# Performance work log

Hardware: AMD Instinct MI355X
Metric: run time of the kernel (lower is better)

## Reference

```python
import jax, jax.numpy as jnp
import numpy as np

IN_FEATURES = 4096
OUT_FEATURES = 11008
LUT_SIZE = 256
N_TOKENS = 64


def setup_inputs() -> dict:
    key = jax.random.key(0)
    k1, k2, k3, k4 = jax.random.split(key, 4)
    x = jax.random.normal(k1, (N_TOKENS, IN_FEATURES), dtype=jnp.float32)
    grid_indices = jax.random.randint(k2, (OUT_FEATURES, IN_FEATURES), 0, LUT_SIZE, dtype=jnp.int32)
    lut = jax.random.normal(k3, (LUT_SIZE,), dtype=jnp.float32)
    scale = jax.random.uniform(k4, (OUT_FEATURES, 1), dtype=jnp.float32)
    return {"x": x, "grid_indices": grid_indices, "lut": lut, "scale": scale}


def reference(x, grid_indices, lut, scale):
    # Dequantize weight: LUT gather per element, then per-output-row scale.
    # weight: [out_features, in_features]
    weight = lut[grid_indices] * scale
    # F.linear(x, W) == x @ W.T ; out: [n_tokens, out_features]
    return jnp.einsum('ti,oi->to', x, weight)
```

## Files before the change

### kernel.cpp

```cpp
#include <hip/hip_runtime.h>
#include <stdint.h>

#define N_TOK 64
#define K_DIM 4096
#define N_OUT 11008
#define LUT_N 256

typedef __attribute__((ext_vector_type(4))) float  floatx4;
typedef __attribute__((ext_vector_type(8))) __bf16 bf16x8;

__device__ __forceinline__ unsigned bf16_rne(float f) {
  unsigned u = __builtin_bit_cast(unsigned, f);
  return (u + 0x7fffu + ((u >> 16) & 1u)) >> 16;
}

__global__ __launch_bounds__(256) void xpack_kernel(const float* __restrict__ x,
                                                    uint32_t* __restrict__ xp) {
  const int t = blockIdx.x * 256 + threadIdx.x;
  const int lane = t & 63, c = t >> 6;
  const int m15 = lane & 15, q = lane >> 4;
  const int tt = c & 3, st = (c >> 2) & 31, w = c >> 7;
  const int src = (tt * 16 + m15) * K_DIM + w * 1024 + st * 32 + q * 8;
  float4 a = *(const float4*)(x + src);
  float4 b = *(const float4*)(x + src + 4);
  uint4 o;
  o.x = bf16_rne(a.x) | (bf16_rne(a.y) << 16);
  o.y = bf16_rne(a.z) | (bf16_rne(a.w) << 16);
  o.z = bf16_rne(b.x) | (bf16_rne(b.y) << 16);
  o.w = bf16_rne(b.z) | (bf16_rne(b.w) << 16);
  *(uint4*)(xp + (size_t)t * 4) = o;
}

__global__ __launch_bounds__(256, 3) void ghost_kernel(
    const int* __restrict__ gidx, const float* __restrict__ lut,
    const float* __restrict__ scale, const uint32_t* __restrict__ xp,
    float* __restrict__ out) {
  __shared__ unsigned lut_lds[LUT_N * 16];
  __shared__ floatx4 red[4][4][64];

  const int tid = threadIdx.x;
  {
    unsigned hb = bf16_rne(lut[tid]);
#pragma unroll
    for (int c = 0; c < 16; ++c) lut_lds[tid * 16 + c] = hb;
  }
  __syncthreads();

  const int w = tid >> 6, lane = tid & 63;
  const int m15 = lane & 15, q = lane >> 4;
  const int o = blockIdx.x * 16 + m15;

  const int* idxp = gidx + (size_t)o * K_DIM + w * 1024 + q * 8;
  const uint4* ap = (const uint4*)xp + (size_t)w * 32 * 4 * 64 + lane;

  floatx4 acc[4];
#pragma unroll
  for (int tt = 0; tt < 4; ++tt) acc[tt] = (floatx4){0.f, 0.f, 0.f, 0.f};

  int4  ib[4][2];
  uint4 ab[4][4];
#pragma unroll
  for (int p = 0; p < 4; ++p) {
    ib[p][0] = *(const int4*)(idxp + p * 32);
    ib[p][1] = *(const int4*)(idxp + p * 32 + 4);
#pragma unroll
    for (int tt = 0; tt < 4; ++tt) ab[p][tt] = ap[(p * 4 + tt) * 64];
  }

#pragma unroll 4
  for (int st = 0; st < 32; ++st) {
    const int p = st & 3;
    const int4 i0 = ib[p][0], i1 = ib[p][1];
    uint4 a0 = ab[p][0], a1 = ab[p][1], a2 = ab[p][2], a3 = ab[p][3];
    if (st < 28) {
      ib[p][0] = *(const int4*)(idxp + (st + 4) * 32);
      ib[p][1] = *(const int4*)(idxp + (st + 4) * 32 + 4);
#pragma unroll
      for (int tt = 0; tt < 4; ++tt) ab[p][tt] = ap[((st + 4) * 4 + tt) * 64];
    }

    unsigned g0 = lut_lds[i0.x * 16 + m15];
    unsigned g1 = lut_lds[i0.y * 16 + m15];
    unsigned g2 = lut_lds[i0.z * 16 + m15];
    unsigned g3 = lut_lds[i0.w * 16 + m15];
    unsigned g4 = lut_lds[i1.x * 16 + m15];
    unsigned g5 = lut_lds[i1.y * 16 + m15];
    unsigned g6 = lut_lds[i1.z * 16 + m15];
    unsigned g7 = lut_lds[i1.w * 16 + m15];
    uint4 bi;
    bi.x = __builtin_amdgcn_perm(g1, g0, 0x05040100u);
    bi.y = __builtin_amdgcn_perm(g3, g2, 0x05040100u);
    bi.z = __builtin_amdgcn_perm(g5, g4, 0x05040100u);
    bi.w = __builtin_amdgcn_perm(g7, g6, 0x05040100u);
    const bf16x8 bfrag = __builtin_bit_cast(bf16x8, bi);

    acc[0] = __builtin_amdgcn_mfma_f32_16x16x32_bf16(
        __builtin_bit_cast(bf16x8, a0), bfrag, acc[0], 0, 0, 0);
    acc[1] = __builtin_amdgcn_mfma_f32_16x16x32_bf16(
        __builtin_bit_cast(bf16x8, a1), bfrag, acc[1], 0, 0, 0);
    acc[2] = __builtin_amdgcn_mfma_f32_16x16x32_bf16(
        __builtin_bit_cast(bf16x8, a2), bfrag, acc[2], 0, 0, 0);
    acc[3] = __builtin_amdgcn_mfma_f32_16x16x32_bf16(
        __builtin_bit_cast(bf16x8, a3), bfrag, acc[3], 0, 0, 0);
  }

  __syncthreads();
#pragma unroll
  for (int tt = 0; tt < 4; ++tt) red[w][tt][lane] = acc[tt];
  __syncthreads();
  {
    floatx4 r = red[0][w][lane];
    r += red[1][w][lane];
    r += red[2][w][lane];
    r += red[3][w][lane];
    const float sc = scale[blockIdx.x * 16 + m15];
    r *= sc;
#pragma unroll
    for (int i = 0; i < 4; ++i)
      out[(size_t)(16 * w + q * 4 + i) * N_OUT + blockIdx.x * 16 + m15] = r[i];
  }
}

extern "C" void kernel_launch(void* const* d_in, const int* in_sizes, int n_in,
                              void* d_out, int out_size, void* d_ws, size_t ws_size,
                              hipStream_t stream) {
  const float* x   = (const float*)d_in[0];
  const int*   gi  = (const int*)d_in[1];
  const float* lut = (const float*)d_in[2];
  const float* sc  = (const float*)d_in[3];
  float*       out = (float*)d_out;

  uint32_t* xp = (uint32_t*)d_ws;
  xpack_kernel<<<(N_TOK * K_DIM / 8) / 256, 256, 0, stream>>>(x, xp);
  ghost_kernel<<<N_OUT / 16, 256, 0, stream>>>(gi, lut, sc, xp, out);
}
```

Before: 273.6 us.

## Stage index tiles into LDS via async global_load_lds double buffering

Grid indices are no longer loaded straight into registers with strided per-row int4 loads. They are now copied per 256-column window into a double-buffered padded LDS tile using global_load_lds, with fully coalesced 1KB row segments. The K split across warps changes from contiguous quarters to interleaved 64-column chunks inside each window, and the x packing layout is changed to a plain k-step order to match. This adds a __syncthreads per window and removes the register prefetch of activation fragments, which risks exposing global latency for the x loads.

```diff
diff --git a/kernel.cpp b/kernel.cpp
--- a/kernel.cpp
+++ b/kernel.cpp
@@ -5,6 +5,8 @@
 #define K_DIM 4096
 #define N_OUT 11008
 #define LUT_N 256
+#define WIN 256
+#define ROWPAD 260
 
 typedef __attribute__((ext_vector_type(4))) float  floatx4;
 typedef __attribute__((ext_vector_type(8))) __bf16 bf16x8;
@@ -19,8 +21,8 @@
   const int t = blockIdx.x * 256 + threadIdx.x;
   const int lane = t & 63, c = t >> 6;
   const int m15 = lane & 15, q = lane >> 4;
-  const int tt = c & 3, st = (c >> 2) & 31, w = c >> 7;
-  const int src = (tt * 16 + m15) * K_DIM + w * 1024 + st * 32 + q * 8;
+  const int tt = c & 3, kstep = c >> 2;
+  const int src = (tt * 16 + m15) * K_DIM + kstep * 32 + q * 8;
   float4 a = *(const float4*)(x + src);
   float4 b = *(const float4*)(x + src + 4);
   uint4 o;
@@ -35,89 +37,100 @@
     const int* __restrict__ gidx, const float* __restrict__ lut,
     const float* __restrict__ scale, const uint32_t* __restrict__ xp,
     float* __restrict__ out) {
-  __shared__ unsigned lut_lds[LUT_N * 16];
-  __shared__ floatx4 red[4][4][64];
+  __shared__ uint32_t lut_lds[LUT_N * 16];
+  __shared__ uint32_t win[2][16 * ROWPAD];
 
   const int tid = threadIdx.x;
+  const int w = tid >> 6, lane = tid & 63;
+  const int m15 = lane & 15, q = lane >> 4;
+  const int blk = blockIdx.x;
+
+  const int* grow = gidx + (size_t)blk * 16 * K_DIM;
+
+  auto load_win = [&](int n) {
+    uint32_t* dst = &win[n & 1][0];
+#pragma unroll
+    for (int j = 0; j < 4; ++j) {
+      const int r = 4 * w + j;
+      const int* g = grow + (size_t)r * K_DIM + n * WIN + lane * 4;
+      __builtin_amdgcn_global_load_lds(
+          (const __attribute__((address_space(1))) void*)g,
+          (__attribute__((address_space(3))) void*)(dst + r * ROWPAD), 16, 0, 0);
+    }
+  };
+
+  load_win(0);
+
   {
     unsigned hb = bf16_rne(lut[tid]);
 #pragma unroll
     for (int c = 0; c < 16; ++c) lut_lds[tid * 16 + c] = hb;
   }
-  __syncthreads();
-
-  const int w = tid >> 6, lane = tid & 63;
-  const int m15 = lane & 15, q = lane >> 4;
-  const int o = blockIdx.x * 16 + m15;
-
-  const int* idxp = gidx + (size_t)o * K_DIM + w * 1024 + q * 8;
-  const uint4* ap = (const uint4*)xp + (size_t)w * 32 * 4 * 64 + lane;
 
   floatx4 acc[4];
 #pragma unroll
   for (int tt = 0; tt < 4; ++tt) acc[tt] = (floatx4){0.f, 0.f, 0.f, 0.f};
 
-  int4  ib[4][2];
-  uint4 ab[4][4];
+  const uint4* ap = (const uint4*)xp;
+
+  for (int n = 0; n < 16; ++n) {
+    __syncthreads();
+    if (n < 15) load_win(n + 1);
+    const uint32_t* wb = &win[n & 1][0];
+    const int kb = n * 8 + w * 2;
+
 #pragma unroll
-  for (int p = 0; p < 4; ++p) {
-    ib[p][0] = *(const int4*)(idxp + p * 32);
-    ib[p][1] = *(const int4*)(idxp + p * 32 + 4);
-#pragma unroll
-    for (int tt = 0; tt < 4; ++tt) ab[p][tt] = ap[(p * 4 + tt) * 64];
-  }
+    for (int s = 0; s < 2; ++s) {
+      uint4 a0 = ap[(size_t)((kb + s) * 4 + 0) * 64 + lane];
+      uint4 a1 = ap[(size_t)((kb + s) * 4 + 1) * 64 + lane];
+      uint4 a2 = ap[(size_t)((kb + s) * 4 + 2) * 64 + lane];
+      uint4 a3 = ap[(size_t)((kb + s) * 4 + 3) * 64 + lane];
 
-#pragma unroll 4
-  for (int st = 0; st < 32; ++st) {
-    const int p = st & 3;
-    const int4 i0 = ib[p][0], i1 = ib[p][1];
-    uint4 a0 = ab[p][0], a1 = ab[p][1], a2 = ab[p][2], a3 = ab[p][3];
-    if (st < 28) {
-      ib[p][0] = *(const int4*)(idxp + (st + 4) * 32);
-      ib[p][1] = *(const int4*)(idxp + (st + 4) * 32 + 4);
-#pragma unroll
-      for (int tt = 0; tt < 4; ++tt) ab[p][tt] = ap[((st + 4) * 4 + tt) * 64];
+      const uint32_t* ip = wb + m15 * ROWPAD + w * 64 + s * 32 + q * 8;
+      const uint4 iv0 = *(const uint4*)ip;
+      const uint4 iv1 = *(const uint4*)(ip + 4);
+
+      unsigned g0 = lut_lds[iv0.x * 16 + m15];
+      unsigned g1 = lut_lds[iv0.y * 16 + m15];
+      unsigned g2 = lut_lds[iv0.z * 16 + m15];
+      unsigned g3 = lut_lds[iv0.w * 16 + m15];
+      unsigned g4 = lut_lds[iv1.x * 16 + m15];
+      unsigned g5 = lut_lds[iv1.y * 16 + m15];
+      unsigned g6 = lut_lds[iv1.z * 16 + m15];
+      unsigned g7 = lut_lds[iv1.w * 16 + m15];
+      uint4 bi;
+      bi.x = __builtin_amdgcn_perm(g1, g0, 0x05040100u);
+      bi.y = __builtin_amdgcn_perm(g3, g2, 0x05040100u);
+      bi.z = __builtin_amdgcn_perm(g5, g4, 0x05040100u);
+      bi.w = __builtin_amdgcn_perm(g7, g6, 0x05040100u);
+      const bf16x8 bfrag = __builtin_bit_cast(bf16x8, bi);
+
+      acc[0] = __builtin_amdgcn_mfma_f32_16x16x32_bf16(
+          __builtin_bit_cast(bf16x8, a0), bfrag, acc[0], 0, 0, 0);
+      acc[1] = __builtin_amdgcn_mfma_f32_16x16x32_bf16(
+          __builtin_bit_cast(bf16x8, a1), bfrag, acc[1], 0, 0, 0);
+      acc[2] = __builtin_amdgcn_mfma_f32_16x16x32_bf16(
+          __builtin_bit_cast(bf16x8, a2), bfrag, acc[2], 0, 0, 0);
+      acc[3] = __builtin_amdgcn_mfma_f32_16x16x32_bf16(
+          __builtin_bit_cast(bf16x8, a3), bfrag, acc[3], 0, 0, 0);
     }
-
-    unsigned g0 = lut_lds[i0.x * 16 + m15];
-    unsigned g1 = lut_lds[i0.y * 16 + m15];
-    unsigned g2 = lut_lds[i0.z * 16 + m15];
-    unsigned g3 = lut_lds[i0.w * 16 + m15];
-    unsigned g4 = lut_lds[i1.x * 16 + m15];
-    unsigned g5 = lut_lds[i1.y * 16 + m15];
-    unsigned g6 = lut_lds[i1.z * 16 + m15];
-    unsigned g7 = lut_lds[i1.w * 16 + m15];
-    uint4 bi;
-    bi.x = __builtin_amdgcn_perm(g1, g0, 0x05040100u);
-    bi.y = __builtin_amdgcn_perm(g3, g2, 0x05040100u);
-    bi.z = __builtin_amdgcn_perm(g5, g4, 0x05040100u);
-    bi.w = __builtin_amdgcn_perm(g7, g6, 0x05040100u);
-    const bf16x8 bfrag = __builtin_bit_cast(bf16x8, bi);
-
-    acc[0] = __builtin_amdgcn_mfma_f32_16x16x32_bf16(
-        __builtin_bit_cast(bf16x8, a0), bfrag, acc[0], 0, 0, 0);
-    acc[1] = __builtin_amdgcn_mfma_f32_16x16x32_bf16(
-        __builtin_bit_cast(bf16x8, a1), bfrag, acc[1], 0, 0, 0);
-    acc[2] = __builtin_amdgcn_mfma_f32_16x16x32_bf16(
-        __builtin_bit_cast(bf16x8, a2), bfrag, acc[2], 0, 0, 0);
-    acc[3] = __builtin_amdgcn_mfma_f32_16x16x32_bf16(
-        __builtin_bit_cast(bf16x8, a3), bfrag, acc[3], 0, 0, 0);
   }
 
   __syncthreads();
+  floatx4* red = (floatx4*)&win[0][0];
 #pragma unroll
-  for (int tt = 0; tt < 4; ++tt) red[w][tt][lane] = acc[tt];
+  for (int tt = 0; tt < 4; ++tt) red[(w * 4 + tt) * 64 + lane] = acc[tt];
   __syncthreads();
   {
-    floatx4 r = red[0][w][lane];
-    r += red[1][w][lane];
-    r += red[2][w][lane];
-    r += red[3][w][lane];
-    const float sc = scale[blockIdx.x * 16 + m15];
+    floatx4 r = red[(0 * 4 + w) * 64 + lane];
+    r += red[(1 * 4 + w) * 64 + lane];
+    r += red[(2 * 4 + w) * 64 + lane];
+    r += red[(3 * 4 + w) * 64 + lane];
+    const float sc = scale[blk * 16 + m15];
     r *= sc;
 #pragma unroll
     for (int i = 0; i < 4; ++i)
-      out[(size_t)(16 * w + q * 4 + i) * N_OUT + blockIdx.x * 16 + m15] = r[i];
+      out[(size_t)(16 * w + q * 4 + i) * N_OUT + blk * 16 + m15] = r[i];
   }
 }
 
```

New measurement: 252.9 us. 1.08x faster.

## Split LUT dequantization into separate kernel writing bf16 weight tiles before GEMM

Applied to the files above, without the earlier changes.

Splits the fused dequant-GEMM into two kernels. The first gathers LUT values for all indices and writes a bf16 weight buffer in MFMA fragment order to workspace. The second is a plain bf16 GEMM that reads that buffer, and the x packing layout changes to match. The aim is to take LDS gathers and permutes out of the MFMA loop, at the cost of an extra write and read of a roughly 90 MB bf16 weight buffer plus one more launch.

```diff
diff --git a/kernel.cpp b/kernel.cpp
--- a/kernel.cpp
+++ b/kernel.cpp
@@ -19,8 +19,8 @@
   const int t = blockIdx.x * 256 + threadIdx.x;
   const int lane = t & 63, c = t >> 6;
   const int m15 = lane & 15, q = lane >> 4;
-  const int tt = c & 3, st = (c >> 2) & 31, w = c >> 7;
-  const int src = (tt * 16 + m15) * K_DIM + w * 1024 + st * 32 + q * 8;
+  const int tt = c & 3, kstep = c >> 2;
+  const int src = (tt * 16 + m15) * K_DIM + kstep * 32 + q * 8;
   float4 a = *(const float4*)(x + src);
   float4 b = *(const float4*)(x + src + 4);
   uint4 o;
@@ -31,69 +31,82 @@
   *(uint4*)(xp + (size_t)t * 4) = o;
 }
 
-__global__ __launch_bounds__(256, 3) void ghost_kernel(
-    const int* __restrict__ gidx, const float* __restrict__ lut,
-    const float* __restrict__ scale, const uint32_t* __restrict__ xp,
-    float* __restrict__ out) {
-  __shared__ unsigned lut_lds[LUT_N * 16];
+__global__ __launch_bounds__(256) void dequant_kernel(const int* __restrict__ gi,
+                                                      const float* __restrict__ lut,
+                                                      uint4* __restrict__ wt) {
+  __shared__ uint32_t lut_lds[LUT_N * 16];
+  {
+    unsigned hb = bf16_rne(lut[threadIdx.x]);
+#pragma unroll
+    for (int c = 0; c < 16; ++c) lut_lds[threadIdx.x * 16 + c] = hb;
+  }
+  __syncthreads();
+
+  const int slot = threadIdx.x & 15;
+  const size_t t = (size_t)blockIdx.x * 256 + threadIdx.x;
+  const int o = (int)(t >> 9);
+  const int kc = (int)(t & 511);
+
+  const int4* p = (const int4*)(gi + ((size_t)o << 12) + (kc << 3));
+  const int4 a = p[0], b = p[1];
+
+  unsigned g0 = lut_lds[a.x * 16 + slot];
+  unsigned g1 = lut_lds[a.y * 16 + slot];
+  unsigned g2 = lut_lds[a.z * 16 + slot];
+  unsigned g3 = lut_lds[a.w * 16 + slot];
+  unsigned g4 = lut_lds[b.x * 16 + slot];
+  unsigned g5 = lut_lds[b.y * 16 + slot];
+  unsigned g6 = lut_lds[b.z * 16 + slot];
+  unsigned g7 = lut_lds[b.w * 16 + slot];
+  uint4 u;
+  u.x = __builtin_amdgcn_perm(g1, g0, 0x05040100u);
+  u.y = __builtin_amdgcn_perm(g3, g2, 0x05040100u);
+  u.z = __builtin_amdgcn_perm(g5, g4, 0x05040100u);
+  u.w = __builtin_amdgcn_perm(g7, g6, 0x05040100u);
+
+  const int to = o >> 4, m = o & 15, tk = kc >> 2, q = kc & 3;
+  wt[((size_t)to * 128 + tk) * 64 + m * 4 + q] = u;
+}
+
+__global__ __launch_bounds__(256, 3) void gemm_kernel(
+    const uint4* __restrict__ wt, const uint32_t* __restrict__ xp,
+    const float* __restrict__ scale, float* __restrict__ out) {
   __shared__ floatx4 red[4][4][64];
 
   const int tid = threadIdx.x;
-  {
-    unsigned hb = bf16_rne(lut[tid]);
-#pragma unroll
-    for (int c = 0; c < 16; ++c) lut_lds[tid * 16 + c] = hb;
-  }
-  __syncthreads();
-
   const int w = tid >> 6, lane = tid & 63;
   const int m15 = lane & 15, q = lane >> 4;
-  const int o = blockIdx.x * 16 + m15;
 
-  const int* idxp = gidx + (size_t)o * K_DIM + w * 1024 + q * 8;
-  const uint4* ap = (const uint4*)xp + (size_t)w * 32 * 4 * 64 + lane;
+  const uint4* bp = wt + (size_t)blockIdx.x * 128 * 64 + m15 * 4 + q;
+  const uint4* ap = (const uint4*)xp + lane;
 
   floatx4 acc[4];
 #pragma unroll
   for (int tt = 0; tt < 4; ++tt) acc[tt] = (floatx4){0.f, 0.f, 0.f, 0.f};
 
-  int4  ib[4][2];
+  uint4 bb[4];
   uint4 ab[4][4];
 #pragma unroll
   for (int p = 0; p < 4; ++p) {
-    ib[p][0] = *(const int4*)(idxp + p * 32);
-    ib[p][1] = *(const int4*)(idxp + p * 32 + 4);
+    bb[p] = bp[(size_t)(w * 32 + p) * 64];
 #pragma unroll
-    for (int tt = 0; tt < 4; ++tt) ab[p][tt] = ap[(p * 4 + tt) * 64];
+    for (int tt = 0; tt < 4; ++tt)
+      ab[p][tt] = ap[(size_t)((w * 32 + p) * 4 + tt) * 64];
   }
 
 #pragma unroll 4
   for (int st = 0; st < 32; ++st) {
     const int p = st & 3;
-    const int4 i0 = ib[p][0], i1 = ib[p][1];
+    const uint4 bv = bb[p];
     uint4 a0 = ab[p][0], a1 = ab[p][1], a2 = ab[p][2], a3 = ab[p][3];
     if (st < 28) {
-      ib[p][0] = *(const int4*)(idxp + (st + 4) * 32);
-      ib[p][1] = *(const int4*)(idxp + (st + 4) * 32 + 4);
+      bb[p] = bp[(size_t)(w * 32 + st + 4) * 64];
 #pragma unroll
-      for (int tt = 0; tt < 4; ++tt) ab[p][tt] = ap[((st + 4) * 4 + tt) * 64];
+      for (int tt = 0; tt < 4; ++tt)
+        ab[p][tt] = ap[(size_t)((w * 32 + st + 4) * 4 + tt) * 64];
     }
 
-    unsigned g0 = lut_lds[i0.x * 16 + m15];
-    unsigned g1 = lut_lds[i0.y * 16 + m15];
-    unsigned g2 = lut_lds[i0.z * 16 + m15];
-    unsigned g3 = lut_lds[i0.w * 16 + m15];
-    unsigned g4 = lut_lds[i1.x * 16 + m15];
-    unsigned g5 = lut_lds[i1.y * 16 + m15];
-    unsigned g6 = lut_lds[i1.z * 16 + m15];
-    unsigned g7 = lut_lds[i1.w * 16 + m15];
-    uint4 bi;
-    bi.x = __builtin_amdgcn_perm(g1, g0, 0x05040100u);
-    bi.y = __builtin_amdgcn_perm(g3, g2, 0x05040100u);
-    bi.z = __builtin_amdgcn_perm(g5, g4, 0x05040100u);
-    bi.w = __builtin_amdgcn_perm(g7, g6, 0x05040100u);
-    const bf16x8 bfrag = __builtin_bit_cast(bf16x8, bi);
-
+    const bf16x8 bfrag = __builtin_bit_cast(bf16x8, bv);
     acc[0] = __builtin_amdgcn_mfma_f32_16x16x32_bf16(
         __builtin_bit_cast(bf16x8, a0), bfrag, acc[0], 0, 0, 0);
     acc[1] = __builtin_amdgcn_mfma_f32_16x16x32_bf16(
@@ -131,6 +144,9 @@
   float*       out = (float*)d_out;
 
   uint32_t* xp = (uint32_t*)d_ws;
+  uint4*    wt = (uint4*)((uint8_t*)d_ws + (1u << 20));
+
   xpack_kernel<<<(N_TOK * K_DIM / 8) / 256, 256, 0, stream>>>(x, xp);
-  ghost_kernel<<<N_OUT / 16, 256, 0, stream>>>(gi, lut, sc, xp, out);
+  dequant_kernel<<<(N_OUT * K_DIM / 8) / 256, 256, 0, stream>>>(gi, lut, wt);
+  gemm_kernel<<<N_OUT / 16, 256, 0, stream>>>(wt, xp, sc, out);
 }
```

Result: slower. 303.8 us (+11.0%).
